# Optimization experiments

Hardware: AMD Instinct MI355X
Metric: run time of the kernel (lower is better)

## Reference

```python
import jax, jax.numpy as jnp
import numpy as np

DIM = 2048
HV = 32          # num value heads
HK = 16          # num key heads
DK = 128         # head_k_dim
DV = 128         # head_v_dim
KW = 4           # conv kernel width
KEY_DIM = HK * DK            # 2048
VAL_DIM = HV * DV            # 4096
CONV_DIM = 2 * KEY_DIM + VAL_DIM  # 8192
EPS = 1e-6
B, T = 2, 2048


def setup_inputs() -> dict:
    key = jax.random.key(0)
    ks = jax.random.split(key, 10)
    s = 0.02
    x = jax.random.normal(ks[0], (B, T, DIM), jnp.float32)
    W_qkv = jax.random.normal(ks[1], (DIM, CONV_DIM), jnp.float32) * s
    W_z = jax.random.normal(ks[2], (DIM, VAL_DIM), jnp.float32) * s
    W_a = jax.random.normal(ks[3], (DIM, HV), jnp.float32) * s
    W_b = jax.random.normal(ks[4], (DIM, HV), jnp.float32) * s
    W_out = jax.random.normal(ks[5], (VAL_DIM, DIM), jnp.float32) * s
    conv_w = jax.random.normal(ks[6], (CONV_DIM, KW), jnp.float32) * 0.2
    A_log = jnp.log(jax.random.uniform(ks[7], (HV,), jnp.float32, 1e-3, 16.0))
    dt_bias = jnp.ones((HV,), jnp.float32)
    norm_weight = jnp.ones((DV,), jnp.float32)
    return {"x": x, "W_qkv": W_qkv, "W_z": W_z, "W_a": W_a, "W_b": W_b,
            "W_out": W_out, "conv_w": conv_w, "dt_bias": dt_bias,
            "A_log": A_log, "norm_weight": norm_weight}


def _l2norm(t):
    return t * jax.lax.rsqrt(jnp.sum(t * t, axis=-1, keepdims=True) + EPS)


def _forward(x, W_qkv, W_z, W_a, W_b, W_out, conv_w, dt_bias, A_log, norm_weight):
    Bb, Tt, _ = x.shape
    mixed = x @ W_qkv                       # [B,T,CONV_DIM]
    z = x @ W_z                             # [B,T,VAL_DIM]
    a = x @ W_a                             # [B,T,HV]
    b = x @ W_b                             # [B,T,HV]

    # depthwise causal conv1d (left pad KW-1) + silu
    xp = jnp.pad(mixed, ((0, 0), (KW - 1, 0), (0, 0)))
    conv = sum(xp[:, i:i + Tt, :] * conv_w[:, i] for i in range(KW))
    mixed = jax.nn.silu(conv)

    q, k, v = jnp.split(mixed, [KEY_DIM, 2 * KEY_DIM], axis=-1)
    q = q.reshape(Bb, Tt, HK, DK)
    k = k.reshape(Bb, Tt, HK, DK)
    v = v.reshape(Bb, Tt, HV, DV)
    rep = HV // HK
    q = jnp.repeat(q, rep, axis=2)          # [B,T,HV,DK]
    k = jnp.repeat(k, rep, axis=2)

    # decay / beta
    beta = jax.nn.sigmoid(b)                                    # [B,T,HV]
    g = -jnp.exp(A_log) * jax.nn.softplus(a + dt_bias)          # [B,T,HV], < 0

    # qk l2norm in kernel + scale
    q = _l2norm(q) * (DK ** -0.5)
    k = _l2norm(k)

    # gated delta rule recurrence, time-major scan
    qT = q.transpose(1, 0, 2, 3)
    kT = k.transpose(1, 0, 2, 3)
    vT = v.transpose(1, 0, 2, 3)
    gT = g.transpose(1, 0, 2)
    bT = beta.transpose(1, 0, 2)
    S0 = jnp.zeros((Bb, HV, DK, DV), jnp.float32)

    def step(S, inp):
        qt, kt, vt, gt, bt = inp
        S = S * jnp.exp(gt)[..., None, None]
        pred = jnp.einsum('bhk,bhkv->bhv', kt, S)
        u = (vt - pred) * bt[..., None]
        S = S + jnp.einsum('bhk,bhv->bhkv', kt, u)
        o = jnp.einsum('bhk,bhkv->bhv', qt, S)
        return S, o

    _, oT = jax.lax.scan(step, S0, (qT, kT, vT, gT, bT))
    o = oT.transpose(1, 0, 2, 3)            # [B,T,HV,DV]

    # gated RMSNorm over head_v_dim: weight * rmsnorm(o) * silu(z)
    var = jnp.mean(o * o, axis=-1, keepdims=True)
    on = o * jax.lax.rsqrt(var + EPS) * norm_weight
    zg = z.reshape(Bb, Tt, HV, DV)
    on = on * jax.nn.silu(zg)

    return on.reshape(Bb, Tt, VAL_DIM) @ W_out


def reference(x, W_qkv, W_z, W_a, W_b, W_out, conv_w, dt_bias, A_log, norm_weight):
    return _forward(x, W_qkv, W_z, W_a, W_b, W_out, conv_w, dt_bias, A_log, norm_weight)
```

## Files before the change

kernel.cpp:

```cpp
#include <hip/hip_runtime.h>
#include <hip/hip_bf16.h>
#include <cstdint>
#include <cstddef>

#define DIM_ 2048
#define HV_ 32
#define HK_ 16
#define DK_ 128
#define DV_ 128
#define KW_ 4
#define KEY_DIM_ 2048
#define VAL_DIM_ 4096
#define CONV_DIM_ 8192
#define B_ 2
#define T_ 2048
#define BT_ 4096
#define CH_ 64
#define NC_ (T_ / CH_)

typedef short s8v __attribute__((ext_vector_type(8)));
typedef float f4v __attribute__((ext_vector_type(4)));

__device__ __forceinline__ unsigned short f2b(float f) {
    union { float f; unsigned u; } c; c.f = f;
    unsigned u = c.u;
    return (unsigned short)((u + 0x7fffu + ((u >> 16) & 1u)) >> 16);
}
__device__ __forceinline__ float b2f(unsigned short s) {
    union { unsigned u; float f; } c; c.u = ((unsigned)s) << 16;
    return c.f;
}
__device__ __forceinline__ unsigned int pk2(float a, float b) {
    return (unsigned)f2b(a) | ((unsigned)f2b(b) << 16);
}
__device__ __forceinline__ float silu(float x) { return x / (1.f + expf(-x)); }

__global__ void cast_bf16_k(const float* __restrict__ in, unsigned short* __restrict__ out, int n8) {
    int i = blockIdx.x * blockDim.x + threadIdx.x;
    if (i >= n8) return;
    int base = i * 8;
    f4v a = *(const f4v*)(in + base);
    f4v b = *(const f4v*)(in + base + 4);
    s8v o;
    o[0] = (short)f2b(a[0]); o[1] = (short)f2b(a[1]); o[2] = (short)f2b(a[2]); o[3] = (short)f2b(a[3]);
    o[4] = (short)f2b(b[0]); o[5] = (short)f2b(b[1]); o[6] = (short)f2b(b[2]); o[7] = (short)f2b(b[3]);
    *(s8v*)(out + base) = o;
}

__global__ void transpose_cast_k(const float* __restrict__ in, unsigned short* __restrict__ out,
                                 int R, int C) {
    __shared__ float tile[32][33];
    int c0 = blockIdx.x * 32, r0 = blockIdx.y * 32;
    int tx = threadIdx.x & 31, ty = threadIdx.x >> 5;
#pragma unroll
    for (int j = 0; j < 32; j += 8)
        tile[ty + j][tx] = in[(size_t)(r0 + ty + j) * C + c0 + tx];
    __syncthreads();
#pragma unroll
    for (int j = 0; j < 32; j += 8)
        out[(size_t)(c0 + ty + j) * R + r0 + tx] = f2b(tile[tx][ty + j]);
}

template <int OUT_BF16>
__global__ __launch_bounds__(256) void gemm_bt_k(const unsigned short* __restrict__ A,
                                                 const unsigned short* __restrict__ BT,
                                                 void* __restrict__ Cv,
                                                 int M, int N, int K) {
    __shared__ __attribute__((aligned(16))) unsigned short As[128 * 64];
    __shared__ __attribute__((aligned(16))) unsigned short Bs[128 * 64];
    const int tid = threadIdx.x;
    const int wid = tid >> 6, lane = tid & 63;
    const int wm = wid >> 1, wn = wid & 1;
    const int m0 = blockIdx.y * 128, n0 = blockIdx.x * 128;

    f4v acc[4][4];
#pragma unroll
    for (int i = 0; i < 4; i++)
#pragma unroll
        for (int j = 0; j < 4; j++) acc[i][j] = (f4v){0.f, 0.f, 0.f, 0.f};

    const int rowA = tid >> 3;
    const int cb   = (tid & 7) << 4;

    for (int kt = 0; kt < K; kt += 64) {
#pragma unroll
        for (int i = 0; i < 4; i++) {
            int row = i * 32 + rowA;
            int scb = cb ^ ((row & 7) << 4);
            const unsigned short* ga = A  + (size_t)(m0 + row) * K + kt + (scb >> 1);
            const unsigned short* gb = BT + (size_t)(n0 + row) * K + kt + (scb >> 1);
            char* la = (char*)As + i * 4096 + (wid << 10);
            char* lb = (char*)Bs + i * 4096 + (wid << 10);
            __builtin_amdgcn_global_load_lds(
                (const __attribute__((address_space(1))) unsigned int*)ga,
                (__attribute__((address_space(3))) unsigned int*)la, 16, 0, 0);
            __builtin_amdgcn_global_load_lds(
                (const __attribute__((address_space(1))) unsigned int*)gb,
                (__attribute__((address_space(3))) unsigned int*)lb, 16, 0, 0);
        }
        __syncthreads();
#pragma unroll
        for (int kk = 0; kk < 2; kk++) {
            s8v af[4], bfr[4];
#pragma unroll
            for (int mi = 0; mi < 4; mi++) {
                int row = wm * 64 + mi * 16 + (lane & 15);
                int byteoff = (row << 7) + ((kk * 64 + ((lane >> 4) << 4)) ^ ((row & 7) << 4));
                af[mi] = *(const s8v*)((const char*)As + byteoff);
            }
#pragma unroll
            for (int ni = 0; ni < 4; ni++) {
                int row = wn * 64 + ni * 16 + (lane & 15);
                int byteoff = (row << 7) + ((kk * 64 + ((lane >> 4) << 4)) ^ ((row & 7) << 4));
                bfr[ni] = *(const s8v*)((const char*)Bs + byteoff);
            }
#pragma unroll
            for (int mi = 0; mi < 4; mi++)
#pragma unroll
                for (int ni = 0; ni < 4; ni++)
                    acc[mi][ni] = __builtin_amdgcn_mfma_f32_16x16x32_bf16(
                        af[mi], bfr[ni], acc[mi][ni], 0, 0, 0);
        }
        __syncthreads();
    }
#pragma unroll
    for (int mi = 0; mi < 4; mi++) {
#pragma unroll
        for (int ni = 0; ni < 4; ni++) {
            int row = m0 + wm * 64 + mi * 16 + ((lane >> 4) << 2);
            int col = n0 + wn * 64 + ni * 16 + (lane & 15);
#pragma unroll
            for (int r = 0; r < 4; r++) {
                float v = acc[mi][ni][r];
                if (OUT_BF16)
                    ((unsigned short*)Cv)[(size_t)(row + r) * N + col] = f2b(v);
                else
                    ((float*)Cv)[(size_t)(row + r) * N + col] = v;
            }
        }
    }
}

__global__ __launch_bounds__(256) void ab_gbeta_k(const float* __restrict__ x,
                                                  const float* __restrict__ Wa,
                                                  const float* __restrict__ Wb,
                                                  const float* __restrict__ dt_bias,
                                                  const float* __restrict__ A_log,
                                                  float* __restrict__ g, float* __restrict__ beta) {
    __shared__ float xr0[16 * 513];
    const int tid = threadIdx.x;
    const int r = tid & 15, cc = tid >> 4;
    const int row0 = blockIdx.x * 16;
    float a0 = 0.f, a1 = 0.f, b0 = 0.f, b1 = 0.f;
    for (int kc = 0; kc < 2048; kc += 512) {
#pragma unroll
        for (int q = 0; q < 8; q++) {
            int f = q * 256 + tid;
            int rw = f >> 7, cl = (f & 127) << 2;
            *(f4v*)&xr0[rw * 513 + cl] = *(const f4v*)(x + (size_t)(row0 + rw) * 2048 + kc + cl);
        }
        __syncthreads();
#pragma unroll 8
        for (int k = 0; k < 512; k++) {
            float xv = xr0[r * 513 + k];
            size_t kk = (size_t)(kc + k) * 32;
            a0 += xv * Wa[kk + cc];
            a1 += xv * Wa[kk + cc + 16];
            b0 += xv * Wb[kk + cc];
            b1 += xv * Wb[kk + cc + 16];
        }
        __syncthreads();
    }
    int row = row0 + r;
    float av0 = a0 + dt_bias[cc], av1 = a1 + dt_bias[cc + 16];
    float sp0 = (av0 > 20.f) ? av0 : log1pf(expf(av0));
    float sp1 = (av1 > 20.f) ? av1 : log1pf(expf(av1));
    g[(size_t)row * 32 + cc]      = -expf(A_log[cc]) * sp0;
    g[(size_t)row * 32 + cc + 16] = -expf(A_log[cc + 16]) * sp1;
    beta[(size_t)row * 32 + cc]      = 1.f / (1.f + expf(-b0));
    beta[(size_t)row * 32 + cc + 16] = 1.f / (1.f + expf(-b1));
}

__global__ __launch_bounds__(256) void conv_fused_k(const unsigned short* __restrict__ mixp,
                                                    const float* __restrict__ convw,
                                                    unsigned short* __restrict__ qn,
                                                    unsigned short* __restrict__ kn,
                                                    unsigned short* __restrict__ vv) {
    int btid = blockIdx.x;
    int t = btid & (T_ - 1);
    int c = (blockIdx.y << 9) + (threadIdx.x << 1);
    const unsigned short* base = mixp + (size_t)btid * CONV_DIM_ + c;
    unsigned m3 = *(const unsigned*)(base);
    unsigned m2 = (t >= 1) ? *(const unsigned*)(base - CONV_DIM_) : 0u;
    unsigned m1 = (t >= 2) ? *(const unsigned*)(base - 2 * CONV_DIM_) : 0u;
    unsigned m0 = (t >= 3) ? *(const unsigned*)(base - 3 * CONV_DIM_) : 0u;
    f4v w0 = *(const f4v*)(convw + (size_t)c * 4);
    f4v w1 = *(const f4v*)(convw + (size_t)c * 4 + 4);
    float v0 = b2f((unsigned short)(m3 & 0xffff)) * w0[3] + b2f((unsigned short)(m2 & 0xffff)) * w0[2]
             + b2f((unsigned short)(m1 & 0xffff)) * w0[1] + b2f((unsigned short)(m0 & 0xffff)) * w0[0];
    float v1 = b2f((unsigned short)(m3 >> 16)) * w1[3] + b2f((unsigned short)(m2 >> 16)) * w1[2]
             + b2f((unsigned short)(m1 >> 16)) * w1[1] + b2f((unsigned short)(m0 >> 16)) * w1[0];
    v0 = silu(v0); v1 = silu(v1);
    if (c < 2 * KEY_DIM_) {
        float ss = v0 * v0 + v1 * v1;
#pragma unroll
        for (int m = 1; m < 64; m <<= 1) ss += __shfl_xor(ss, m);
        float scale = rsqrtf(ss + 1e-6f);
        int head = (c >> 7) & 15, d = c & 127;
        if (c < KEY_DIM_) {
            scale *= 0.08838834764831845f;
            *(unsigned*)(qn + ((size_t)btid * HK_ + head) * DK_ + d) = pk2(v0 * scale, v1 * scale);
        } else {
            *(unsigned*)(kn + ((size_t)btid * HK_ + head) * DK_ + d) = pk2(v0 * scale, v1 * scale);
        }
    } else {
        *(unsigned*)(vv + (size_t)btid * VAL_DIM_ + (c - 2 * KEY_DIM_)) = pk2(v0, v1);
    }
}

__global__ __launch_bounds__(256) void chunk_pre_k(
    const unsigned short* __restrict__ qn, const unsigned short* __restrict__ kn,
    unsigned short* __restrict__ vv,
    const float* __restrict__ g, const float* __restrict__ beta,
    unsigned short* __restrict__ Wg, unsigned short* __restrict__ Aog,
    unsigned short* __restrict__ knT, float* __restrict__ expG, float* __restrict__ expGr)
{
    const int c = blockIdx.x, h = blockIdx.y, b = blockIdx.z;
    const int hk = h >> 1;
    const int tid = threadIdx.x, wid = tid >> 6, lane = tid & 63;
    const int r15 = lane & 15, g4 = lane >> 4;

    __shared__ __attribute__((aligned(16))) unsigned short Klds[64 * 128];
    __shared__ __attribute__((aligned(16))) unsigned short Xlds[128 * 64];
    __shared__ float AT[64][68];
    __shared__ float STmp[16][17];
    __shared__ float Gl[64], Bl[64], EG[64];

    const size_t t0 = (size_t)b * T_ + (size_t)c * 64;
    const size_t cbk = ((size_t)(b * 32 + h) * 32 + c);

#pragma unroll
    for (int p = 0; p < 4; p++) {
        int row = p * 16 + (tid >> 4);
        int colB = (tid & 15) << 4;
        int sw = colB ^ ((row & 7) << 4);
        s8v kv = *(const s8v*)(kn + ((t0 + row) * HK_ + hk) * DK_ + (colB >> 1));
        *(s8v*)((char*)Klds + row * 256 + sw) = kv;
        s8v qv = *(const s8v*)(qn + ((t0 + row) * HK_ + hk) * DK_ + (colB >> 1));
        *(s8v*)((char*)Xlds + row * 256 + sw) = qv;
    }
    if (tid < 64) {
        Gl[tid] = g[(t0 + tid) * HV_ + h];
        Bl[tid] = beta[(t0 + tid) * HV_ + h];
    }
    __syncthreads();
    if (tid == 0) {
        float s = 0.f;
        for (int i = 0; i < 64; i++) { s += Gl[i]; Gl[i] = s; }
    }
    __syncthreads();
    if (tid < 64) {
        float Gi = Gl[tid], Gn = Gl[63];
        float e1 = expf(Gi), e2 = expf(Gn - Gi);
        EG[tid] = e1;
        expG[cbk * 64 + tid] = e1;
        expGr[cbk * 64 + tid] = e2;
    }
    __syncthreads();

    f4v kkv[4], qkv[4];
#pragma unroll
    for (int jt = 0; jt < 4; jt++) { kkv[jt] = (f4v){0,0,0,0}; qkv[jt] = (f4v){0,0,0,0}; }
    const int arow = wid * 16 + r15;
#pragma unroll
    for (int ks = 0; ks < 4; ks++) {
        int abyte = arow * 256 + ((ks * 64 + (g4 << 4)) ^ ((arow & 7) << 4));
        s8v ak = *(const s8v*)((const char*)Klds + abyte);
        s8v aq = *(const s8v*)((const char*)Xlds + abyte);
#pragma unroll
        for (int jt = 0; jt < 4; jt++) {
            int jrow = jt * 16 + r15;
            int bbyte = jrow * 256 + ((ks * 64 + (g4 << 4)) ^ ((jrow & 7) << 4));
            s8v bk = *(const s8v*)((const char*)Klds + bbyte);
            kkv[jt] = __builtin_amdgcn_mfma_f32_16x16x32_bf16(ak, bk, kkv[jt], 0, 0, 0);
            qkv[jt] = __builtin_amdgcn_mfma_f32_16x16x32_bf16(aq, bk, qkv[jt], 0, 0, 0);
        }
    }
#pragma unroll
    for (int jt = 0; jt < 4; jt++) {
#pragma unroll
        for (int r = 0; r < 4; r++) {
            int i = wid * 16 + g4 * 4 + r;
            int j = jt * 16 + r15;
            float em = expf(fminf(Gl[i] - Gl[j], 0.f));
            AT[i][j] = (j < i) ? Bl[i] * em * kkv[jt][r] : 0.f;
            float ao = (j <= i) ? em * qkv[jt][r] : 0.f;
            Aog[cbk * 4096 + i * 64 + j] = f2b(ao);
        }
    }
    __syncthreads();

    for (int u = tid; u < 1024; u += 256) {
        int row = u >> 4, v0i = (u & 15) << 3;
        s8v vx = *(const s8v*)(vv + (t0 + row) * VAL_DIM_ + h * 128 + v0i);
        float bt = Bl[row];
#pragma unroll
        for (int e = 0; e < 8; e++) {
            int v = v0i + e;
            *(unsigned short*)((char*)Xlds + v * 128 + ((row * 2) ^ ((v & 7) << 4))) =
                f2b(b2f((unsigned short)vx[e]) * bt);
        }
    }
    if ((h & 1) == 0) {
        int dk = tid & 127, th = (tid >> 7) << 5;
        size_t basek = ((size_t)(b * 16 + hk) * 128 + dk) * (size_t)T_ + (size_t)c * 64 + th;
#pragma unroll
        for (int t8 = 0; t8 < 4; t8++) {
            s8v kv;
#pragma unroll
            for (int e = 0; e < 8; e++) {
                int tt = th + t8 * 8 + e;
                kv[e] = (short)*(const unsigned short*)((const char*)Klds + tt * 256 + ((dk * 2) ^ ((tt & 7) << 4)));
            }
            *(s8v*)(knT + basek + t8 * 8) = kv;
        }
    }
    __syncthreads();

    if (lane < 16) {
        int r0 = wid * 16, col = lane;
#pragma unroll
        for (int i = 0; i < 16; i++) {
            float s = 0.f;
            for (int j = 0; j < i; j++) s += AT[r0 + i][r0 + j] * AT[r0 + j][r0 + col];
            AT[r0 + i][r0 + col] = ((col == i) ? 1.f : 0.f) - s;
        }
    }
    __syncthreads();

    {
        int ii = tid >> 4, jj = tid & 15;
        for (int I = 1; I < 4; I++)
            for (int J = 0; J < I; J++) {
                float s = 0.f;
                for (int K = J; K < I; K++) {
#pragma unroll
                    for (int m = 0; m < 16; m++)
                        s += AT[16 * I + ii][16 * K + m] * AT[16 * K + m][16 * J + jj];
                }
                STmp[ii][jj] = s;
                __syncthreads();
                float y = 0.f;
#pragma unroll
                for (int m = 0; m < 16; m++) y += AT[16 * I + ii][16 * I + m] * STmp[m][jj];
                __syncthreads();
                AT[16 * I + ii][16 * J + jj] = -y;
                __syncthreads();
            }
    }

    f4v tb[8];
#pragma unroll
    for (int vt = 0; vt < 8; vt++) tb[vt] = (f4v){0,0,0,0};
#pragma unroll
    for (int ks = 0; ks < 2; ks++) {
        s8v ta;
#pragma unroll
        for (int e = 0; e < 8; e++) ta[e] = (short)f2b(AT[arow][ks * 32 + g4 * 8 + e]);
#pragma unroll
        for (int vt = 0; vt < 8; vt++) {
            int v = vt * 16 + r15;
            int bbyte = v * 128 + ((ks * 64 + (g4 << 4)) ^ ((v & 7) << 4));
            s8v bv = *(const s8v*)((const char*)Xlds + bbyte);
            tb[vt] = __builtin_amdgcn_mfma_f32_16x16x32_bf16(ta, bv, tb[vt], 0, 0, 0);
        }
    }
#pragma unroll
    for (int vt = 0; vt < 8; vt++)
#pragma unroll
        for (int r = 0; r < 4; r++) {
            int i = wid * 16 + g4 * 4 + r, v = vt * 16 + r15;
            vv[(t0 + i) * VAL_DIM_ + h * 128 + v] = f2b(tb[vt][r]);
        }
    __syncthreads();

    {
        int dk = tid & 127;
        int tb0 = (tid >> 7) << 5;
#pragma unroll
        for (int t8 = 0; t8 < 4; t8++) {
            int tbase = tb0 + t8 * 8;
            s8v kw;
#pragma unroll
            for (int e = 0; e < 8; e++) {
                int t = tbase + e;
                float kv = b2f(*(const unsigned short*)((const char*)Klds + t * 256 + ((dk * 2) ^ ((t & 7) << 4))));
                kw[e] = (short)f2b(kv * Bl[t] * EG[t]);
            }
            *(s8v*)((char*)Xlds + dk * 128 + ((tbase * 2) ^ ((dk & 7) << 4))) = kw;
        }
    }
    __syncthreads();

    f4v wm[8];
#pragma unroll
    for (int dt = 0; dt < 8; dt++) wm[dt] = (f4v){0,0,0,0};
#pragma unroll
    for (int ks = 0; ks < 2; ks++) {
        s8v ta;
#pragma unroll
        for (int e = 0; e < 8; e++) ta[e] = (short)f2b(AT[arow][ks * 32 + g4 * 8 + e]);
#pragma unroll
        for (int dt = 0; dt < 8; dt++) {
            int dkr = dt * 16 + r15;
            int bbyte = dkr * 128 + ((ks * 64 + (g4 << 4)) ^ ((dkr & 7) << 4));
            s8v bw = *(const s8v*)((const char*)Xlds + bbyte);
            wm[dt] = __builtin_amdgcn_mfma_f32_16x16x32_bf16(ta, bw, wm[dt], 0, 0, 0);
        }
    }
#pragma unroll
    for (int dt = 0; dt < 8; dt++)
#pragma unroll
        for (int r = 0; r < 4; r++) {
            int i = wid * 16 + g4 * 4 + r, dk = dt * 16 + r15;
            Wg[cbk * 8192 + i * 128 + dk] = f2b(wm[dt][r]);
        }
}

__global__ __launch_bounds__(256) void chunk_scan_k(
    const unsigned short* __restrict__ qn, const unsigned short* __restrict__ knT,
    const unsigned short* __restrict__ tbv,
    const unsigned short* __restrict__ Wg, const unsigned short* __restrict__ Aog,
    const float* __restrict__ expG, const float* __restrict__ expGr,
    unsigned short* __restrict__ ob)
{
    const int bx = blockIdx.x;
    const int vq = bx & 3, h = (bx >> 2) & 31, b = bx >> 7;
    const int hk = h >> 1;
    const int tid = threadIdx.x, wid = tid >> 6, lane = tid & 63;
    const int r15 = lane & 15, g4 = lane >> 4;

    __shared__ __attribute__((aligned(16))) unsigned short Slds[32 * 128];
    __shared__ __attribute__((aligned(16))) unsigned short Ulds[32 * 64];
    __shared__ __attribute__((aligned(16))) unsigned short Uplds[32 * 64];

    f4v S[2][2];
#pragma unroll
    for (int i = 0; i < 2; i++)
#pragma unroll
        for (int j = 0; j < 2; j++) S[i][j] = (f4v){0,0,0,0};

    for (int c = 0; c < NC_; c++) {
        const size_t cbk = ((size_t)(b * 32 + h) * 32 + c);
        const size_t t0 = (size_t)b * T_ + (size_t)c * 64;

#pragma unroll
        for (int dkt = 0; dkt < 2; dkt++)
#pragma unroll
            for (int vt = 0; vt < 2; vt++) {
                int v = vt * 16 + r15;
                int dkb = ((wid * 2 + dkt) * 16 + g4 * 4) * 2;
                int sw = (v & 7) << 4;
                *(unsigned int*)((char*)Slds + v * 256 + ((dkb) ^ sw))     = pk2(S[dkt][vt][0], S[dkt][vt][1]);
                *(unsigned int*)((char*)Slds + v * 256 + ((dkb + 4) ^ sw)) = pk2(S[dkt][vt][2], S[dkt][vt][3]);
            }
        __syncthreads();

        f4v P[2]; P[0] = (f4v){0,0,0,0}; P[1] = (f4v){0,0,0,0};
        s8v sf[4][2];
        const unsigned short* wp = Wg + cbk * 8192 + (size_t)(wid * 16 + r15) * 128;
#pragma unroll
        for (int ks = 0; ks < 4; ks++) {
            s8v aw = *(const s8v*)(wp + ks * 32 + g4 * 8);
#pragma unroll
            for (int vt = 0; vt < 2; vt++) {
                int v = vt * 16 + r15;
                sf[ks][vt] = *(const s8v*)((const char*)Slds + v * 256 + ((ks * 64 + g4 * 16) ^ ((v & 7) << 4)));
                P[vt] = __builtin_amdgcn_mfma_f32_16x16x32_bf16(aw, sf[ks][vt], P[vt], 0, 0, 0);
            }
        }
        float egr[4];
#pragma unroll
        for (int r = 0; r < 4; r++) egr[r] = expGr[cbk * 64 + wid * 16 + g4 * 4 + r];
#pragma unroll
        for (int vt = 0; vt < 2; vt++) {
            float uu[4], up[4];
#pragma unroll
            for (int r = 0; r < 4; r++) {
                int t = wid * 16 + g4 * 4 + r;
                unsigned short tv = tbv[(t0 + t) * VAL_DIM_ + h * 128 + vq * 32 + vt * 16 + r15];
                uu[r] = b2f(tv) - P[vt][r];
                up[r] = uu[r] * egr[r];
            }
            int v = vt * 16 + r15;
            int tb2 = (wid * 16 + g4 * 4) * 2;
            int sw = (v & 7) << 4;
            *(unsigned int*)((char*)Ulds  + v * 128 + ((tb2) ^ sw))     = pk2(uu[0], uu[1]);
            *(unsigned int*)((char*)Ulds  + v * 128 + ((tb2 + 4) ^ sw)) = pk2(uu[2], uu[3]);
            *(unsigned int*)((char*)Uplds + v * 128 + ((tb2) ^ sw))     = pk2(up[0], up[1]);
            *(unsigned int*)((char*)Uplds + v * 128 + ((tb2 + 4) ^ sw)) = pk2(up[2], up[3]);
        }
        __syncthreads();

        f4v O[2]; O[0] = (f4v){0,0,0,0}; O[1] = (f4v){0,0,0,0};
        float egi = expG[cbk * 64 + wid * 16 + r15];
        const unsigned short* qp = qn + ((t0 + wid * 16 + r15) * HK_ + hk) * DK_;
#pragma unroll
        for (int ks = 0; ks < 4; ks++) {
            s8v q0 = *(const s8v*)(qp + ks * 32 + g4 * 8);
            s8v qg;
#pragma unroll
            for (int e = 0; e < 8; e++) qg[e] = (short)f2b(b2f((unsigned short)q0[e]) * egi);
#pragma unroll
            for (int vt = 0; vt < 2; vt++)
                O[vt] = __builtin_amdgcn_mfma_f32_16x16x32_bf16(qg, sf[ks][vt], O[vt], 0, 0, 0);
        }
        const unsigned short* ap = Aog + cbk * 4096 + (size_t)(wid * 16 + r15) * 64;
#pragma unroll
        for (int ks = 0; ks < 2; ks++) {
            s8v aa = *(const s8v*)(ap + ks * 32 + g4 * 8);
#pragma unroll
            for (int vt = 0; vt < 2; vt++) {
                int v = vt * 16 + r15;
                s8v bu = *(const s8v*)((const char*)Ulds + v * 128 + ((ks * 64 + g4 * 16) ^ ((v & 7) << 4)));
                O[vt] = __builtin_amdgcn_mfma_f32_16x16x32_bf16(aa, bu, O[vt], 0, 0, 0);
            }
        }
#pragma unroll
        for (int vt = 0; vt < 2; vt++)
#pragma unroll
            for (int r = 0; r < 4; r++) {
                int t = c * 64 + wid * 16 + g4 * 4 + r;
                ob[((size_t)b * T_ + t) * VAL_DIM_ + h * 128 + vq * 32 + vt * 16 + r15] = f2b(O[vt][r]);
            }

        float gam = expG[cbk * 64 + 63];
#pragma unroll
        for (int dkt = 0; dkt < 2; dkt++)
#pragma unroll
            for (int vt = 0; vt < 2; vt++) {
                S[dkt][vt][0] *= gam; S[dkt][vt][1] *= gam;
                S[dkt][vt][2] *= gam; S[dkt][vt][3] *= gam;
            }
        const unsigned short* kp = knT + ((size_t)(b * 16 + hk) * 128) * (size_t)T_;
#pragma unroll
        for (int ks = 0; ks < 2; ks++) {
            s8v bu[2];
#pragma unroll
            for (int vt = 0; vt < 2; vt++) {
                int v = vt * 16 + r15;
                bu[vt] = *(const s8v*)((const char*)Uplds + v * 128 + ((ks * 64 + g4 * 16) ^ ((v & 7) << 4)));
            }
#pragma unroll
            for (int dkt = 0; dkt < 2; dkt++) {
                s8v ak = *(const s8v*)(kp + (size_t)((wid * 2 + dkt) * 16 + r15) * T_ + (size_t)c * 64 + ks * 32 + g4 * 8);
#pragma unroll
                for (int vt = 0; vt < 2; vt++)
                    S[dkt][vt] = __builtin_amdgcn_mfma_f32_16x16x32_bf16(ak, bu[vt], S[dkt][vt], 0, 0, 0);
            }
        }
        __syncthreads();
    }
}

__global__ __launch_bounds__(256) void norm_gate_k(unsigned short* __restrict__ o,
                                                   const unsigned short* __restrict__ z,
                                                   const float* __restrict__ nw) {
    int lane = threadIdx.x & 63;
    size_t bh = (size_t)blockIdx.x * 4 + (threadIdx.x >> 6);
    unsigned ov = *(unsigned*)(o + bh * 128 + lane * 2);
    float v0 = b2f((unsigned short)(ov & 0xffff)), v1 = b2f((unsigned short)(ov >> 16));
    float ss = v0 * v0 + v1 * v1;
#pragma unroll
    for (int m = 1; m < 64; m <<= 1) ss += __shfl_xor(ss, m);
    float rr = rsqrtf(ss * (1.f / 128.f) + 1e-6f);
    unsigned zv = *(const unsigned*)(z + bh * 128 + lane * 2);
    float z0 = b2f((unsigned short)(zv & 0xffff)), z1 = b2f((unsigned short)(zv >> 16));
    float o0 = v0 * rr * nw[lane * 2]     * silu(z0);
    float o1 = v1 * rr * nw[lane * 2 + 1] * silu(z1);
    *(unsigned*)(o + bh * 128 + lane * 2) = pk2(o0, o1);
}

extern "C" void kernel_launch(void* const* d_in, const int* in_sizes, int n_in,
                              void* d_out, int out_size, void* d_ws, size_t ws_size,
                              hipStream_t stream) {
    const float* x      = (const float*)d_in[0];
    const float* W_qkv  = (const float*)d_in[1];
    const float* W_z    = (const float*)d_in[2];
    const float* W_a    = (const float*)d_in[3];
    const float* W_b    = (const float*)d_in[4];
    const float* W_out  = (const float*)d_in[5];
    const float* conv_w = (const float*)d_in[6];
    const float* dt_bias= (const float*)d_in[7];
    const float* A_log  = (const float*)d_in[8];
    const float* norm_w = (const float*)d_in[9];

    char* w = (char*)d_ws;
    const size_t MBc = (size_t)1 << 20;
    unsigned short* mixp  = (unsigned short*)(w);
    unsigned short* Wmat  = (unsigned short*)(w);
    unsigned short* knT   = (unsigned short*)(w + 32 * MBc);
    unsigned short* Aog   = (unsigned short*)(w + 48 * MBc);
    unsigned short* WqkvT = (unsigned short*)(w + 64 * MBc);
    unsigned short* obuf  = (unsigned short*)(w + 64 * MBc);
    unsigned short* kn    = (unsigned short*)(w + 80 * MBc);
    unsigned short* WzT   = (unsigned short*)(w + 96 * MBc);
    unsigned short* WoutT = (unsigned short*)(w + 96 * MBc);
    unsigned short* xb    = (unsigned short*)(w + 112 * MBc);
    unsigned short* qn    = (unsigned short*)(w + 112 * MBc);
    unsigned short* vv    = (unsigned short*)(w + 128 * MBc);
    unsigned short* zb    = (unsigned short*)(w + 160 * MBc);
    float* gbuf  = (float*)(w + 192 * MBc);
    float* bbuf  = (float*)(w + 192 * MBc + 512 * 1024);
    float* expG  = (float*)(w + 192 * MBc + 1024 * 1024);
    float* expGr = (float*)(w + 192 * MBc + 1536 * 1024);

    cast_bf16_k<<<(BT_ * DIM_ / 8 + 255) / 256, 256, 0, stream>>>(x, xb, BT_ * DIM_ / 8);
    transpose_cast_k<<<dim3(CONV_DIM_ / 32, DIM_ / 32), 256, 0, stream>>>(W_qkv, WqkvT, DIM_, CONV_DIM_);
    transpose_cast_k<<<dim3(VAL_DIM_ / 32, DIM_ / 32), 256, 0, stream>>>(W_z, WzT, DIM_, VAL_DIM_);
    gemm_bt_k<1><<<dim3(CONV_DIM_ / 128, BT_ / 128), 256, 0, stream>>>(xb, WqkvT, mixp, BT_, CONV_DIM_, DIM_);
    gemm_bt_k<1><<<dim3(VAL_DIM_ / 128, BT_ / 128), 256, 0, stream>>>(xb, WzT, zb, BT_, VAL_DIM_, DIM_);
    transpose_cast_k<<<dim3(DIM_ / 32, VAL_DIM_ / 32), 256, 0, stream>>>(W_out, WoutT, VAL_DIM_, DIM_);
    ab_gbeta_k<<<BT_ / 16, 256, 0, stream>>>(x, W_a, W_b, dt_bias, A_log, gbuf, bbuf);
    conv_fused_k<<<dim3(BT_, CONV_DIM_ / 512), 256, 0, stream>>>(mixp, conv_w, qn, kn, vv);
    chunk_pre_k<<<dim3(NC_, HV_, B_), 256, 0, stream>>>(qn, kn, vv, gbuf, bbuf,
                                                        Wmat, Aog, knT, expG, expGr);
    chunk_scan_k<<<B_ * HV_ * 4, 256, 0, stream>>>(qn, knT, vv, Wmat, Aog, expG, expGr, obuf);
    norm_gate_k<<<BT_ * HV_ / 4, 256, 0, stream>>>(obuf, zb, norm_w);
    gemm_bt_k<0><<<dim3(DIM_ / 128, BT_ / 128), 256, 0, stream>>>(obuf, WoutT, d_out, BT_, DIM_, VAL_DIM_);
}
```

Before: 754.2 us.

## Split chunk scan over 8 value slices and fuse x bf16 cast into ab_gbeta

The chunk scan now launches 8 blocks per (batch, head), each owning 16 value columns instead of 32, which doubles the number of blocks working on the serial recurrence and halves per-block state and LDS. The barrier placement inside the chunk loop is rearranged: the trailing barrier is removed and one is added after the q·S MFMAs, before the U tile is read back. The separate bf16 cast kernel for x is removed, and the cast is done inside ab_gbeta_k while it already loads x, saving one pass over x. In exchange, each smaller block does less MFMA work per load of Wg, Aog, knT and q, so redundant global reads of those operands across value slices roughly double.

```diff
diff --git a/kernel.cpp b/kernel.cpp
--- a/kernel.cpp
+++ b/kernel.cpp
@@ -35,18 +35,6 @@
 }
 __device__ __forceinline__ float silu(float x) { return x / (1.f + expf(-x)); }
 
-__global__ void cast_bf16_k(const float* __restrict__ in, unsigned short* __restrict__ out, int n8) {
-    int i = blockIdx.x * blockDim.x + threadIdx.x;
-    if (i >= n8) return;
-    int base = i * 8;
-    f4v a = *(const f4v*)(in + base);
-    f4v b = *(const f4v*)(in + base + 4);
-    s8v o;
-    o[0] = (short)f2b(a[0]); o[1] = (short)f2b(a[1]); o[2] = (short)f2b(a[2]); o[3] = (short)f2b(a[3]);
-    o[4] = (short)f2b(b[0]); o[5] = (short)f2b(b[1]); o[6] = (short)f2b(b[2]); o[7] = (short)f2b(b[3]);
-    *(s8v*)(out + base) = o;
-}
-
 __global__ void transpose_cast_k(const float* __restrict__ in, unsigned short* __restrict__ out,
                                  int R, int C) {
     __shared__ float tile[32][33];
@@ -146,7 +134,8 @@
                                                   const float* __restrict__ Wb,
                                                   const float* __restrict__ dt_bias,
                                                   const float* __restrict__ A_log,
-                                                  float* __restrict__ g, float* __restrict__ beta) {
+                                                  float* __restrict__ g, float* __restrict__ beta,
+                                                  unsigned short* __restrict__ xb) {
     __shared__ float xr0[16 * 513];
     const int tid = threadIdx.x;
     const int r = tid & 15, cc = tid >> 4;
@@ -157,7 +146,11 @@
         for (int q = 0; q < 8; q++) {
             int f = q * 256 + tid;
             int rw = f >> 7, cl = (f & 127) << 2;
-            *(f4v*)&xr0[rw * 513 + cl] = *(const f4v*)(x + (size_t)(row0 + rw) * 2048 + kc + cl);
+            f4v xv = *(const f4v*)(x + (size_t)(row0 + rw) * 2048 + kc + cl);
+            *(f4v*)&xr0[rw * 513 + cl] = xv;
+            unsigned long long p = (unsigned long long)pk2(xv[0], xv[1])
+                                 | ((unsigned long long)pk2(xv[2], xv[3]) << 32);
+            *(unsigned long long*)(xb + (size_t)(row0 + rw) * 2048 + kc + cl) = p;
         }
         __syncthreads();
 #pragma unroll 8
@@ -435,74 +428,60 @@
     unsigned short* __restrict__ ob)
 {
     const int bx = blockIdx.x;
-    const int vq = bx & 3, h = (bx >> 2) & 31, b = bx >> 7;
+    const int vq = bx & 7, h = (bx >> 3) & 31, b = bx >> 8;
     const int hk = h >> 1;
     const int tid = threadIdx.x, wid = tid >> 6, lane = tid & 63;
     const int r15 = lane & 15, g4 = lane >> 4;
 
-    __shared__ __attribute__((aligned(16))) unsigned short Slds[32 * 128];
-    __shared__ __attribute__((aligned(16))) unsigned short Ulds[32 * 64];
-    __shared__ __attribute__((aligned(16))) unsigned short Uplds[32 * 64];
-
-    f4v S[2][2];
-#pragma unroll
-    for (int i = 0; i < 2; i++)
-#pragma unroll
-        for (int j = 0; j < 2; j++) S[i][j] = (f4v){0,0,0,0};
+    __shared__ __attribute__((aligned(16))) unsigned short Slds[16 * 128];
+    __shared__ __attribute__((aligned(16))) unsigned short Ulds[16 * 64];
+    __shared__ __attribute__((aligned(16))) unsigned short Uplds[16 * 64];
+
+    f4v S[2];
+    S[0] = (f4v){0,0,0,0}; S[1] = (f4v){0,0,0,0};
+
+    const int v = r15;
+    const int sw = (v & 7) << 4;
 
     for (int c = 0; c < NC_; c++) {
         const size_t cbk = ((size_t)(b * 32 + h) * 32 + c);
         const size_t t0 = (size_t)b * T_ + (size_t)c * 64;
 
 #pragma unroll
-        for (int dkt = 0; dkt < 2; dkt++)
-#pragma unroll
-            for (int vt = 0; vt < 2; vt++) {
-                int v = vt * 16 + r15;
-                int dkb = ((wid * 2 + dkt) * 16 + g4 * 4) * 2;
-                int sw = (v & 7) << 4;
-                *(unsigned int*)((char*)Slds + v * 256 + ((dkb) ^ sw))     = pk2(S[dkt][vt][0], S[dkt][vt][1]);
-                *(unsigned int*)((char*)Slds + v * 256 + ((dkb + 4) ^ sw)) = pk2(S[dkt][vt][2], S[dkt][vt][3]);
-            }
+        for (int dkt = 0; dkt < 2; dkt++) {
+            int dkb = ((wid * 2 + dkt) * 16 + g4 * 4) * 2;
+            *(unsigned int*)((char*)Slds + v * 256 + ((dkb) ^ sw))     = pk2(S[dkt][0], S[dkt][1]);
+            *(unsigned int*)((char*)Slds + v * 256 + ((dkb + 4) ^ sw)) = pk2(S[dkt][2], S[dkt][3]);
+        }
         __syncthreads();
 
-        f4v P[2]; P[0] = (f4v){0,0,0,0}; P[1] = (f4v){0,0,0,0};
-        s8v sf[4][2];
+        f4v P = (f4v){0,0,0,0};
+        s8v sf[4];
         const unsigned short* wp = Wg + cbk * 8192 + (size_t)(wid * 16 + r15) * 128;
 #pragma unroll
         for (int ks = 0; ks < 4; ks++) {
             s8v aw = *(const s8v*)(wp + ks * 32 + g4 * 8);
-#pragma unroll
-            for (int vt = 0; vt < 2; vt++) {
-                int v = vt * 16 + r15;
-                sf[ks][vt] = *(const s8v*)((const char*)Slds + v * 256 + ((ks * 64 + g4 * 16) ^ ((v & 7) << 4)));
-                P[vt] = __builtin_amdgcn_mfma_f32_16x16x32_bf16(aw, sf[ks][vt], P[vt], 0, 0, 0);
-            }
-        }
-        float egr[4];
-#pragma unroll
-        for (int r = 0; r < 4; r++) egr[r] = expGr[cbk * 64 + wid * 16 + g4 * 4 + r];
-#pragma unroll
-        for (int vt = 0; vt < 2; vt++) {
-            float uu[4], up[4];
-#pragma unroll
-            for (int r = 0; r < 4; r++) {
-                int t = wid * 16 + g4 * 4 + r;
-                unsigned short tv = tbv[(t0 + t) * VAL_DIM_ + h * 128 + vq * 32 + vt * 16 + r15];
-                uu[r] = b2f(tv) - P[vt][r];
-                up[r] = uu[r] * egr[r];
-            }
-            int v = vt * 16 + r15;
-            int tb2 = (wid * 16 + g4 * 4) * 2;
-            int sw = (v & 7) << 4;
-            *(unsigned int*)((char*)Ulds  + v * 128 + ((tb2) ^ sw))     = pk2(uu[0], uu[1]);
-            *(unsigned int*)((char*)Ulds  + v * 128 + ((tb2 + 4) ^ sw)) = pk2(uu[2], uu[3]);
-            *(unsigned int*)((char*)Uplds + v * 128 + ((tb2) ^ sw))     = pk2(up[0], up[1]);
-            *(unsigned int*)((char*)Uplds + v * 128 + ((tb2 + 4) ^ sw)) = pk2(up[2], up[3]);
-        }
-        __syncthreads();
-
-        f4v O[2]; O[0] = (f4v){0,0,0,0}; O[1] = (f4v){0,0,0,0};
+            sf[ks] = *(const s8v*)((const char*)Slds + v * 256 + ((ks * 64 + g4 * 16) ^ sw));
+            P = __builtin_amdgcn_mfma_f32_16x16x32_bf16(aw, sf[ks], P, 0, 0, 0);
+        }
+        float egr4[4];
+#pragma unroll
+        for (int r = 0; r < 4; r++) egr4[r] = expGr[cbk * 64 + wid * 16 + g4 * 4 + r];
+        float uu[4], up[4];
+#pragma unroll
+        for (int r = 0; r < 4; r++) {
+            int t = wid * 16 + g4 * 4 + r;
+            unsigned short tv = tbv[(t0 + t) * VAL_DIM_ + h * 128 + vq * 16 + r15];
+            uu[r] = b2f(tv) - P[r];
+            up[r] = uu[r] * egr4[r];
+        }
+        int tb2 = (wid * 16 + g4 * 4) * 2;
+        *(unsigned int*)((char*)Ulds  + v * 128 + ((tb2) ^ sw))     = pk2(uu[0], uu[1]);
+        *(unsigned int*)((char*)Ulds  + v * 128 + ((tb2 + 4) ^ sw)) = pk2(uu[2], uu[3]);
+        *(unsigned int*)((char*)Uplds + v * 128 + ((tb2) ^ sw))     = pk2(up[0], up[1]);
+        *(unsigned int*)((char*)Uplds + v * 128 + ((tb2 + 4) ^ sw)) = pk2(up[2], up[3]);
+
+        f4v O = (f4v){0,0,0,0};
         float egi = expG[cbk * 64 + wid * 16 + r15];
         const unsigned short* qp = qn + ((t0 + wid * 16 + r15) * HK_ + hk) * DK_;
 #pragma unroll
@@ -511,55 +490,35 @@
             s8v qg;
 #pragma unroll
             for (int e = 0; e < 8; e++) qg[e] = (short)f2b(b2f((unsigned short)q0[e]) * egi);
-#pragma unroll
-            for (int vt = 0; vt < 2; vt++)
-                O[vt] = __builtin_amdgcn_mfma_f32_16x16x32_bf16(qg, sf[ks][vt], O[vt], 0, 0, 0);
-        }
+            O = __builtin_amdgcn_mfma_f32_16x16x32_bf16(qg, sf[ks], O, 0, 0, 0);
+        }
+        __syncthreads();
+
         const unsigned short* ap = Aog + cbk * 4096 + (size_t)(wid * 16 + r15) * 64;
 #pragma unroll
         for (int ks = 0; ks < 2; ks++) {
             s8v aa = *(const s8v*)(ap + ks * 32 + g4 * 8);
-#pragma unroll
-            for (int vt = 0; vt < 2; vt++) {
-                int v = vt * 16 + r15;
-                s8v bu = *(const s8v*)((const char*)Ulds + v * 128 + ((ks * 64 + g4 * 16) ^ ((v & 7) << 4)));
-                O[vt] = __builtin_amdgcn_mfma_f32_16x16x32_bf16(aa, bu, O[vt], 0, 0, 0);
-            }
-        }
-#pragma unroll
-        for (int vt = 0; vt < 2; vt++)
-#pragma unroll
-            for (int r = 0; r < 4; r++) {
-                int t = c * 64 + wid * 16 + g4 * 4 + r;
-                ob[((size_t)b * T_ + t) * VAL_DIM_ + h * 128 + vq * 32 + vt * 16 + r15] = f2b(O[vt][r]);
-            }
+            s8v bu = *(const s8v*)((const char*)Ulds + v * 128 + ((ks * 64 + g4 * 16) ^ sw));
+            O = __builtin_amdgcn_mfma_f32_16x16x32_bf16(aa, bu, O, 0, 0, 0);
+        }
+#pragma unroll
+        for (int r = 0; r < 4; r++) {
+            int t = c * 64 + wid * 16 + g4 * 4 + r;
+            ob[((size_t)b * T_ + t) * VAL_DIM_ + h * 128 + vq * 16 + r15] = f2b(O[r]);
+        }
 
         float gam = expG[cbk * 64 + 63];
-#pragma unroll
-        for (int dkt = 0; dkt < 2; dkt++)
-#pragma unroll
-            for (int vt = 0; vt < 2; vt++) {
-                S[dkt][vt][0] *= gam; S[dkt][vt][1] *= gam;
-                S[dkt][vt][2] *= gam; S[dkt][vt][3] *= gam;
-            }
+        S[0] *= gam; S[1] *= gam;
         const unsigned short* kp = knT + ((size_t)(b * 16 + hk) * 128) * (size_t)T_;
 #pragma unroll
         for (int ks = 0; ks < 2; ks++) {
-            s8v bu[2];
-#pragma unroll
-            for (int vt = 0; vt < 2; vt++) {
-                int v = vt * 16 + r15;
-                bu[vt] = *(const s8v*)((const char*)Uplds + v * 128 + ((ks * 64 + g4 * 16) ^ ((v & 7) << 4)));
-            }
+            s8v bu = *(const s8v*)((const char*)Uplds + v * 128 + ((ks * 64 + g4 * 16) ^ sw));
 #pragma unroll
             for (int dkt = 0; dkt < 2; dkt++) {
                 s8v ak = *(const s8v*)(kp + (size_t)((wid * 2 + dkt) * 16 + r15) * T_ + (size_t)c * 64 + ks * 32 + g4 * 8);
-#pragma unroll
-                for (int vt = 0; vt < 2; vt++)
-                    S[dkt][vt] = __builtin_amdgcn_mfma_f32_16x16x32_bf16(ak, bu[vt], S[dkt][vt], 0, 0, 0);
-            }
-        }
-        __syncthreads();
+                S[dkt] = __builtin_amdgcn_mfma_f32_16x16x32_bf16(ak, bu, S[dkt], 0, 0, 0);
+            }
+        }
     }
 }
 
@@ -615,17 +574,16 @@
     float* expG  = (float*)(w + 192 * MBc + 1024 * 1024);
     float* expGr = (float*)(w + 192 * MBc + 1536 * 1024);
 
-    cast_bf16_k<<<(BT_ * DIM_ / 8 + 255) / 256, 256, 0, stream>>>(x, xb, BT_ * DIM_ / 8);
+    ab_gbeta_k<<<BT_ / 16, 256, 0, stream>>>(x, W_a, W_b, dt_bias, A_log, gbuf, bbuf, xb);
     transpose_cast_k<<<dim3(CONV_DIM_ / 32, DIM_ / 32), 256, 0, stream>>>(W_qkv, WqkvT, DIM_, CONV_DIM_);
     transpose_cast_k<<<dim3(VAL_DIM_ / 32, DIM_ / 32), 256, 0, stream>>>(W_z, WzT, DIM_, VAL_DIM_);
     gemm_bt_k<1><<<dim3(CONV_DIM_ / 128, BT_ / 128), 256, 0, stream>>>(xb, WqkvT, mixp, BT_, CONV_DIM_, DIM_);
     gemm_bt_k<1><<<dim3(VAL_DIM_ / 128, BT_ / 128), 256, 0, stream>>>(xb, WzT, zb, BT_, VAL_DIM_, DIM_);
     transpose_cast_k<<<dim3(DIM_ / 32, VAL_DIM_ / 32), 256, 0, stream>>>(W_out, WoutT, VAL_DIM_, DIM_);
-    ab_gbeta_k<<<BT_ / 16, 256, 0, stream>>>(x, W_a, W_b, dt_bias, A_log, gbuf, bbuf);
     conv_fused_k<<<dim3(BT_, CONV_DIM_ / 512), 256, 0, stream>>>(mixp, conv_w, qn, kn, vv);
     chunk_pre_k<<<dim3(NC_, HV_, B_), 256, 0, stream>>>(qn, kn, vv, gbuf, bbuf,
                                                         Wmat, Aog, knT, expG, expGr);
-    chunk_scan_k<<<B_ * HV_ * 4, 256, 0, stream>>>(qn, knT, vv, Wmat, Aog, expG, expGr, obuf);
+    chunk_scan_k<<<B_ * HV_ * 8, 256, 0, stream>>>(qn, knT, vv, Wmat, Aog, expG, expGr, obuf);
     norm_gate_k<<<BT_ * HV_ / 4, 256, 0, stream>>>(obuf, zb, norm_w);
     gemm_bt_k<0><<<dim3(DIM_ / 128, BT_ / 128), 256, 0, stream>>>(obuf, WoutT, d_out, BT_, DIM_, VAL_DIM_);
 }
```

Result: slower. 781.8 us (+3.7%).
